# Kernel tuning notes

Measured on AMD Instinct MI355X. Metric: run time of the kernel, lower is better.

## Reference

```python
import jax, jax.numpy as jnp
import numpy as np

B, K, NQ = 16, 4, 10  # batch, n_blocks, n_qubits
DIM = 2 ** NQ


def setup_inputs() -> dict:
    key = jax.random.key(0)
    k1, k2 = jax.random.split(key)
    weights = jax.random.normal(k1, (B, K, 1, NQ, 1, 1), dtype=jnp.float32)
    state = jax.random.normal(k2, (B, K, 1, DIM, 1), dtype=jnp.float32)
    return {"weights": weights, "state": state}


def _rx_mats(weights):
    # weights: (B, K, 1, NQ, 1, 1) real angles -> per-qubit Rx 2x2: [[cos, -i sin], [-i sin, cos]]
    w = weights[..., 0, 0]  # (B, K, 1, NQ)
    a = jnp.cos(w / 2).astype(jnp.complex64)
    b = jnp.sin(w / 2).astype(jnp.complex64)
    eye = jnp.eye(2, dtype=jnp.complex64)
    offx = jnp.array([[0.0, 1.0], [1.0, 0.0]], dtype=jnp.complex64)
    return a[..., None, None] * eye - 1j * b[..., None, None] * offx  # (B,K,1,NQ,2,2)


def _kron_chain(rxs):
    # rxs: (B, K, 1, NQ, 2, 2) -> U: (B, K, 1, 2**NQ, 2**NQ)
    U = rxs[..., 0, :, :]
    for q in range(1, rxs.shape[-3]):
        m = U.shape[-1]
        Rq = rxs[..., q, :, :]
        # kron(U, Rq): outer product over matrix indices, then merge
        U = (U[..., :, None, :, None] * Rq[..., None, :, None, :]).reshape(*U.shape[:-2], 2 * m, 2 * m)
    return U


def reference(weights, state):
    U = _kron_chain(_rx_mats(weights))              # (B,K,1,2^n,2^n) complex64
    psi = state.astype(jnp.complex64)               # (B,K,1,2^n,1)
    return jnp.matmul(U, psi)                       # (B,K,1,2^n,1) complex64
```

## Files before the change

### kernel.cpp

```cpp
#include <hip/hip_runtime.h>

constexpr int BK  = 16 * 4;
constexpr int NQ  = 10;
constexpr int DIM = 1 << NQ;

__global__ __launch_bounds__(512)
void rx_layer_kernel(const float* __restrict__ weights,
                     const float* __restrict__ state,
                     float* __restrict__ out_re,
                     float* __restrict__ out_im)
{
    __shared__ float re[DIM];
    __shared__ float im[DIM];

    const int bk = blockIdx.x;
    const int t  = threadIdx.x;

    const float* st = state + bk * DIM;
    re[t]       = st[t];       im[t]       = 0.0f;
    re[t + 512] = st[t + 512]; im[t + 512] = 0.0f;

    const float* w = weights + bk * NQ;

    #pragma unroll
    for (int q = 0; q < NQ; ++q) {
        __syncthreads();
        const float wv = w[q];
        const float a  = cosf(0.5f * wv);
        const float b  = sinf(0.5f * wv);

        const int s  = 1 << (NQ - 1 - q);
        const int i0 = ((t & ~(s - 1)) << 1) | (t & (s - 1));
        const int i1 = i0 + s;

        const float x0r = re[i0], x0i = im[i0];
        const float x1r = re[i1], x1i = im[i1];

        re[i0] = a * x0r + b * x1i;
        im[i0] = a * x0i - b * x1r;
        re[i1] = a * x1r + b * x0i;
        im[i1] = a * x1i - b * x0r;
    }
    __syncthreads();

    float* orr = out_re + bk * DIM;
    orr[t]       = re[t];
    orr[t + 512] = re[t + 512];
    if (out_im != nullptr) {
        float* oi = out_im + bk * DIM;
        oi[t]       = im[t];
        oi[t + 512] = im[t + 512];
    }
}

extern "C" void kernel_launch(void* const* d_in, const int* in_sizes, int n_in,
                              void* d_out, int out_size, void* d_ws, size_t ws_size,
                              hipStream_t stream) {
    const float* weights = (const float*)d_in[0];
    const float* state   = (const float*)d_in[1];
    float* out = (float*)d_out;

    float* out_re = out;
    float* out_im = nullptr;
    if (out_size >= 2 * BK * DIM) {
        out_im = out + BK * DIM;
    }
    rx_layer_kernel<<<BK, 512, 0, stream>>>(weights, state, out_re, out_im);
}
```

Baseline: 57.98 us.

## Keep state in registers of one wavefront, apply gates via shuffles

Each block now has a single 64-lane wavefront that holds all 1024 amplitudes in registers, 16 per lane, loaded and stored as float4. Gates on middle qubits use cross-lane xor shuffles, while gates on the low and high qubits act within each lane's registers. This removes the shared-memory traffic and the ten block-wide barriers. In exchange, each block now runs only 64 threads, so the GPU has much less parallelism across the 64 blocks.

```diff
diff --git a/kernel.cpp b/kernel.cpp
--- a/kernel.cpp
+++ b/kernel.cpp
@@ -1,55 +1,75 @@
 #include <hip/hip_runtime.h>
+
 
 constexpr int BK  = 16 * 4;
 constexpr int NQ  = 10;
 constexpr int DIM = 1 << NQ;
 
-__global__ __launch_bounds__(512)
+__global__ __launch_bounds__(64)
 void rx_layer_kernel(const float* __restrict__ weights,
                      const float* __restrict__ state,
                      float* __restrict__ out_re,
                      float* __restrict__ out_im)
 {
-    __shared__ float re[DIM];
-    __shared__ float im[DIM];
+    const int bk   = blockIdx.x;
+    const int lane = threadIdx.x;
 
-    const int bk = blockIdx.x;
-    const int t  = threadIdx.x;
-
-    const float* st = state + bk * DIM;
-    re[t]       = st[t];       im[t]       = 0.0f;
-    re[t + 512] = st[t + 512]; im[t + 512] = 0.0f;
+    float re[16], im[16];
+    const float4* st4 = reinterpret_cast<const float4*>(state + bk * DIM);
+    #pragma unroll
+    for (int g = 0; g < 4; ++g) {
+        const float4 v = st4[g * 64 + lane];
+        re[g * 4 + 0] = v.x; re[g * 4 + 1] = v.y;
+        re[g * 4 + 2] = v.z; re[g * 4 + 3] = v.w;
+        im[g * 4 + 0] = 0.0f; im[g * 4 + 1] = 0.0f;
+        im[g * 4 + 2] = 0.0f; im[g * 4 + 3] = 0.0f;
+    }
 
     const float* w = weights + bk * NQ;
 
     #pragma unroll
     for (int q = 0; q < NQ; ++q) {
-        __syncthreads();
         const float wv = w[q];
         const float a  = cosf(0.5f * wv);
         const float b  = sinf(0.5f * wv);
+        const int   p  = NQ - 1 - q;
 
-        const int s  = 1 << (NQ - 1 - q);
-        const int i0 = ((t & ~(s - 1)) << 1) | (t & (s - 1));
-        const int i1 = i0 + s;
+        if (p >= 2 && p <= 7) {
+            const int lmask = 1 << (p - 2);
+            #pragma unroll
+            for (int r = 0; r < 16; ++r) {
+                const float pr = __shfl_xor(re[r], lmask);
+                const float pi = __shfl_xor(im[r], lmask);
+                re[r] = a * re[r] + b * pi;
+                im[r] = a * im[r] - b * pr;
+            }
+        } else {
+            const int m = (p >= 8) ? (1 << (p - 6)) : (1 << p);
+            #pragma unroll
+            for (int r0 = 0; r0 < 16; ++r0) {
+                if (r0 & m) continue;
+                const int r1 = r0 | m;
+                const float x0r = re[r0], x0i = im[r0];
+                const float x1r = re[r1], x1i = im[r1];
+                re[r0] = a * x0r + b * x1i;
+                im[r0] = a * x0i - b * x1r;
+                re[r1] = a * x1r + b * x0i;
+                im[r1] = a * x1i - b * x0r;
+            }
+        }
+    }
 
-        const float x0r = re[i0], x0i = im[i0];
-        const float x1r = re[i1], x1i = im[i1];
-
-        re[i0] = a * x0r + b * x1i;
-        im[i0] = a * x0i - b * x1r;
-        re[i1] = a * x1r + b * x0i;
-        im[i1] = a * x1i - b * x0r;
-    }
-    __syncthreads();
-
-    float* orr = out_re + bk * DIM;
-    orr[t]       = re[t];
-    orr[t + 512] = re[t + 512];
+    float4* or4 = reinterpret_cast<float4*>(out_re + bk * DIM);
+    #pragma unroll
+    for (int g = 0; g < 4; ++g)
+        or4[g * 64 + lane] =
+            make_float4(re[g*4+0], re[g*4+1], re[g*4+2], re[g*4+3]);
     if (out_im != nullptr) {
-        float* oi = out_im + bk * DIM;
-        oi[t]       = im[t];
-        oi[t + 512] = im[t + 512];
+        float4* oi4 = reinterpret_cast<float4*>(out_im + bk * DIM);
+        #pragma unroll
+        for (int g = 0; g < 4; ++g)
+            oi4[g * 64 + lane] =
+                make_float4(im[g*4+0], im[g*4+1], im[g*4+2], im[g*4+3]);
     }
 }
 
@@ -65,5 +85,5 @@
     if (out_size >= 2 * BK * DIM) {
         out_im = out + BK * DIM;
     }
-    rx_layer_kernel<<<BK, 512, 0, stream>>>(weights, state, out_re, out_im);
+    rx_layer_kernel<<<BK, 64, 0, stream>>>(weights, state, out_re, out_im);
 }
```

Result: no change. 57.35 us (-1.1%).
